# Kernel optimization log

Hardware: AMD Instinct MI355X
Metric: run time of the kernel (lower is better)

## Reference

```python
import jax, jax.numpy as jnp
import numpy as np

D_MODEL = 768
N_HEADS = 12
HEAD_DIM = D_MODEL // N_HEADS


def setup_inputs() -> dict:
    key = jax.random.key(0)
    ks = jax.random.split(key, 9)
    B, S = 2, 2048
    x = jax.random.normal(ks[0], (B, S, D_MODEL), dtype=jnp.float32)
    s = 1.0 / np.sqrt(D_MODEL)
    Wq = jax.random.normal(ks[1], (D_MODEL, D_MODEL), dtype=jnp.float32) * s
    bq = jax.random.normal(ks[2], (D_MODEL,), dtype=jnp.float32) * 0.01
    Wk = jax.random.normal(ks[3], (D_MODEL, D_MODEL), dtype=jnp.float32) * s
    bk = jax.random.normal(ks[4], (D_MODEL,), dtype=jnp.float32) * 0.01
    Wv = jax.random.normal(ks[5], (D_MODEL, D_MODEL), dtype=jnp.float32) * s
    bv = jax.random.normal(ks[6], (D_MODEL,), dtype=jnp.float32) * 0.01
    Wo = jax.random.normal(ks[7], (D_MODEL, D_MODEL), dtype=jnp.float32) * s
    bo = jax.random.normal(ks[8], (D_MODEL,), dtype=jnp.float32) * 0.01
    return {"x": x, "Wq": Wq, "bq": bq, "Wk": Wk, "bk": bk,
            "Wv": Wv, "bv": bv, "Wo": Wo, "bo": bo}


def reference(x, Wq, bq, Wk, bk, Wv, bv, Wo, bo):
    B, S, _ = x.shape
    H, Dh = N_HEADS, HEAD_DIM
    # Projections (torch Linear: x @ W.T + b; here W stored as [in, out])
    q = (x @ Wq + bq).reshape(B, S, H, Dh)
    k = (x @ Wk + bk).reshape(B, S, H, Dh)
    v = (x @ Wv + bv).reshape(B, S, H, Dh)
    scale = 1.0 / jnp.sqrt(jnp.float32(Dh))
    # NOTE: source applies no causal mask despite the class name.
    scores = jnp.einsum('bqhd,bkhd->bhqk', q, k) * scale
    attn = jax.nn.softmax(scores, axis=-1)
    out = jnp.einsum('bhqk,bkhd->bqhd', attn, v).reshape(B, S, H * Dh)
    return out @ Wo + bo
```

## Files before the change

kernel.cpp:

```cpp
#include <hip/hip_runtime.h>

typedef unsigned short u16;
typedef __fp16 halfx2 __attribute__((ext_vector_type(2)));
typedef __fp16 halfx8 __attribute__((ext_vector_type(8)));
typedef float floatx4 __attribute__((ext_vector_type(4)));
typedef unsigned short u16x4 __attribute__((ext_vector_type(4)));
typedef unsigned short u16x8 __attribute__((ext_vector_type(8)));

#define D_MODEL 768
#define NH 12
#define DH 64
#define SEQ 2048
#define BATCH 2
#define MTOK 4096
#define DQKV 2304

__device__ __forceinline__ u16 f2h(float f) {
    __fp16 h = (__fp16)f;
    return __builtin_bit_cast(u16, h);
}

__device__ __forceinline__ void gload_lds16(const void* g, void* l) {
    __builtin_amdgcn_global_load_lds(
        (const __attribute__((address_space(1))) void*)g,
        (__attribute__((address_space(3))) void*)l, 16, 0, 0);
}


__global__ __launch_bounds__(256) void wprep_kernel(const float* __restrict__ Wq, const float* __restrict__ Wk,
                                                    const float* __restrict__ Wv, const float* __restrict__ Wo,
                                                    const float* __restrict__ x,
                                                    u16* __restrict__ WqkvT, u16* __restrict__ WoT,
                                                    u16* __restrict__ xh) {
    __shared__ u16 t[64][72];
    int bid = blockIdx.x;
    int tid = threadIdx.x;
    if (bid >= 576) {
        int idx = (bid - 576) * 2048 + tid * 8;
        float4 v0 = *(const float4*)(x + idx);
        float4 v1 = *(const float4*)(x + idx + 4);
        union { u16x8 u; halfx2 h[4]; } pk;
        pk.h[0] = __builtin_amdgcn_cvt_pkrtz(v0.x, v0.y);
        pk.h[1] = __builtin_amdgcn_cvt_pkrtz(v0.z, v0.w);
        pk.h[2] = __builtin_amdgcn_cvt_pkrtz(v1.x, v1.y);
        pk.h[3] = __builtin_amdgcn_cvt_pkrtz(v1.z, v1.w);
        *(u16x8*)(xh + idx) = pk.u;
        return;
    }
    int z = bid / 144;
    int t2 = bid % 144;
    int k0 = (t2 / 12) * 64, n0 = (t2 % 12) * 64;
    const float* W = (z == 0) ? Wq : (z == 1) ? Wk : (z == 2) ? Wv : Wo;
    u16* dst = (z < 3) ? (WqkvT + (size_t)z * 768 * 768) : WoT;
#pragma unroll
    for (int p = 0; p < 16; ++p) {
        int idx = p * 256 + tid;
        int kr = idx >> 6, nc = idx & 63;
        t[kr][nc] = f2h(W[(size_t)(k0 + kr) * 768 + n0 + nc]);
    }
    __syncthreads();
#pragma unroll
    for (int p = 0; p < 16; ++p) {
        int idx = p * 256 + tid;
        int nr = idx >> 6, kc = idx & 63;
        dst[(size_t)(n0 + nr) * 768 + k0 + kc] = t[kc][nr];
    }
}


__global__ __launch_bounds__(256) void gemm_qkv(const u16* __restrict__ xh, const u16* __restrict__ Bt,
                                                const float* __restrict__ bq, const float* __restrict__ bk,
                                                const float* __restrict__ bv,
                                                u16* __restrict__ qP, u16* __restrict__ kP,
                                                u16* __restrict__ vTout) {
    const int tid = threadIdx.x;
    const int wid = tid >> 6;
    const int lane = tid & 63;
    const int qd = lane >> 4;
    const int l15 = lane & 15;

    const int tn = blockIdx.x * 128;
    const int tm = blockIdx.y * 64;
    const int wm = (wid >> 1) * 32;
    const int wn = (wid & 1) * 64;

    __shared__ alignas(16) u16 As[64 * 64];
    __shared__ alignas(16) u16 Bs[128 * 64];

    floatx4 acc[2][4];
#pragma unroll
    for (int i = 0; i < 2; ++i)
#pragma unroll
        for (int j = 0; j < 4; ++j) acc[i][j] = (floatx4)(0.0f);

    const u16* Ag[2];
#pragma unroll
    for (int rd = 0; rd < 2; ++rd) {
        int s = rd * 256 + tid;
        int r = s >> 3, bl = (s & 7) ^ (r & 7);
        Ag[rd] = xh + (size_t)(tm + r) * 768 + bl * 8;
    }
    const u16* Bg[4];
#pragma unroll
    for (int rd = 0; rd < 4; ++rd) {
        int s = rd * 256 + tid;
        int r = s >> 3, bl = (s & 7) ^ (r & 7);
        Bg[rd] = Bt + (size_t)(tn + r) * 768 + bl * 8;
    }

    for (int kb = 0; kb < 768; kb += 64) {
        __syncthreads();
#pragma unroll
        for (int rd = 0; rd < 2; ++rd)
            gload_lds16(Ag[rd] + kb, As + (size_t)(rd * 256 + tid) * 8);
#pragma unroll
        for (int rd = 0; rd < 4; ++rd)
            gload_lds16(Bg[rd] + kb, Bs + (size_t)(rd * 256 + tid) * 8);
        __syncthreads();

#pragma unroll
        for (int ks = 0; ks < 2; ++ks) {
            halfx8 af[2], bf[4];
#pragma unroll
            for (int i = 0; i < 2; ++i) {
                int r = wm + i * 16 + l15;
                af[i] = *(const halfx8*)(As + r * 64 + (((ks * 4 + qd) ^ (r & 7)) * 8));
            }
#pragma unroll
            for (int j = 0; j < 4; ++j) {
                int r2 = wn + j * 16 + l15;
                bf[j] = *(const halfx8*)(Bs + r2 * 64 + (((ks * 4 + qd) ^ (r2 & 7)) * 8));
            }
#pragma unroll
            for (int i = 0; i < 2; ++i)
#pragma unroll
                for (int j = 0; j < 4; ++j)
                    acc[i][j] = __builtin_amdgcn_mfma_f32_16x16x32_f16(af[i], bf[j], acc[i][j], 0, 0, 0);
        }
    }

    const float cscale = 0.125f * 1.44269504088896340736f;
    const int rgn = (tn < 768) ? 0 : (tn < 1536) ? 1 : 2;
    const float* bsrc = (rgn == 0) ? bq : (rgn == 1) ? bk : bv;
#pragma unroll
    for (int j = 0; j < 4; ++j) {
        int col = tn + wn + j * 16 + l15;
        int cl = col - rgn * 768;
        float bvv = bsrc[cl];
        int h = cl >> 6, d = cl & 63;
#pragma unroll
        for (int i = 0; i < 2; ++i) {
            int row0 = tm + wm + i * 16 + qd * 4;
            int b = row0 >> 11, s0 = row0 & 2047;
            u16x4 pk;
#pragma unroll
            for (int r = 0; r < 4; ++r) {
                float v = acc[i][j][r] + bvv;
                if (rgn == 0) v *= cscale;
                pk[r] = f2h(v);
            }
            if (rgn == 2) {
                *(u16x4*)(vTout + ((size_t)(b * NH + h) * 64 + d) * SEQ + s0) = pk;
            } else {
                u16* dst = (rgn == 0) ? qP : kP;
#pragma unroll
                for (int r = 0; r < 4; ++r)
                    dst[((size_t)(b * NH + h) * SEQ + s0 + r) * DH + d] = pk[r];
            }
        }
    }
}


__global__ __launch_bounds__(256, 2) void attn_kernel(const u16* __restrict__ qP, const u16* __restrict__ kP,
                                                      const u16* __restrict__ vT, u16* __restrict__ attn) {
    const int tid = threadIdx.x;
    const int wid = tid >> 6;
    const int lane = tid & 63;
    const int qd = lane >> 4;
    const int l15 = lane & 15;

    const int bh = blockIdx.x;
    const int b = bh / NH, h = bh % NH;
    const int q0 = blockIdx.y * 64;

    __shared__ alignas(16) u16 smem[9216];
    u16* ps = smem + wid * 2304;

    halfx8 aq[4][2];
#pragma unroll
    for (int jn = 0; jn < 4; ++jn)
#pragma unroll
        for (int ks = 0; ks < 2; ++ks)
            aq[jn][ks] = *(const halfx8*)(qP + (size_t)(bh * SEQ + q0 + jn * 16 + l15) * DH + ks * 32 + qd * 8);

    halfx8 ones;
#pragma unroll
    for (int j = 0; j < 8; ++j) ones[j] = (__fp16)1.0f;

    floatx4 o[4][4];
#pragma unroll
    for (int ip = 0; ip < 4; ++ip)
#pragma unroll
        for (int jn = 0; jn < 4; ++jn) o[ip][jn] = (floatx4)(0.0f);
    floatx4 lsum[4];
#pragma unroll
    for (int jn = 0; jn < 4; ++jn) lsum[jn] = (floatx4)(0.0f);

    const u16* kbase = kP + (size_t)(bh * SEQ + wid * 32 + l15) * DH + qd * 8;
    const u16* vbase = vT + (size_t)(bh * 64 + l15) * SEQ + wid * 32 + qd * 8;

    halfx8 avA[4], avB[4];
    floatx4 scA[2][4], scB[2][4];
    {
        halfx8 akp[2][2];
#pragma unroll
        for (int mi = 0; mi < 2; ++mi)
#pragma unroll
            for (int ks = 0; ks < 2; ++ks)
                akp[mi][ks] = *(const halfx8*)(kbase + (size_t)(mi * 16) * DH + ks * 32);
#pragma unroll
        for (int ip = 0; ip < 4; ++ip)
            avA[ip] = *(const halfx8*)(vbase + (size_t)(ip * 16) * SEQ);

#pragma unroll
        for (int mi = 0; mi < 2; ++mi)
#pragma unroll
            for (int jn = 0; jn < 4; ++jn) scA[mi][jn] = (floatx4)(0.0f);
#pragma unroll
        for (int ks = 0; ks < 2; ++ks)
#pragma unroll
            for (int mi = 0; mi < 2; ++mi)
#pragma unroll
                for (int jn = 0; jn < 4; ++jn)
                    scA[mi][jn] = __builtin_amdgcn_mfma_f32_16x16x32_f16(akp[mi][ks], aq[jn][ks], scA[mi][jn], 0, 0, 0);
    }

    auto body = [&](int kt,
                    floatx4 (&scC)[2][4], floatx4 (&scN)[2][4],
                    halfx8 (&avU)[4], halfx8 (&avF)[4]) {
        const int kt1 = (kt + 1) & 15;

        halfx8 akn[2][2];
#pragma unroll
        for (int mi = 0; mi < 2; ++mi)
#pragma unroll
            for (int ks = 0; ks < 2; ++ks)
                akn[mi][ks] = *(const halfx8*)(kbase + (size_t)(kt1 * 128 + mi * 16) * DH + ks * 32);
#pragma unroll
        for (int ip = 0; ip < 4; ++ip)
            avF[ip] = *(const halfx8*)(vbase + (size_t)(ip * 16) * SEQ + kt1 * 128);

#pragma unroll
        for (int mi = 0; mi < 2; ++mi)
#pragma unroll
            for (int jn = 0; jn < 4; ++jn) {
                float p0 = __builtin_amdgcn_exp2f(scC[mi][jn][0]);
                float p1 = __builtin_amdgcn_exp2f(scC[mi][jn][1]);
                float p2 = __builtin_amdgcn_exp2f(scC[mi][jn][2]);
                float p3 = __builtin_amdgcn_exp2f(scC[mi][jn][3]);
                union { u16x4 u; halfx2 h[2]; } pk;
                pk.h[0] = __builtin_amdgcn_cvt_pkrtz(p0, p1);
                pk.h[1] = __builtin_amdgcn_cvt_pkrtz(p2, p3);
                *(u16x4*)(ps + (jn * 16 + l15) * 36 + mi * 16 + qd * 4) = pk.u;
            }

#pragma unroll
        for (int mi = 0; mi < 2; ++mi)
#pragma unroll
            for (int jn = 0; jn < 4; ++jn) scN[mi][jn] = (floatx4)(0.0f);
        __builtin_amdgcn_s_setprio(1);
#pragma unroll
        for (int ks = 0; ks < 2; ++ks)
#pragma unroll
            for (int mi = 0; mi < 2; ++mi)
#pragma unroll
                for (int jn = 0; jn < 4; ++jn)
                    scN[mi][jn] = __builtin_amdgcn_mfma_f32_16x16x32_f16(akn[mi][ks], aq[jn][ks], scN[mi][jn], 0, 0, 0);
        __builtin_amdgcn_s_setprio(0);

        halfx8 bp[4];
#pragma unroll
        for (int jn = 0; jn < 4; ++jn) {
            union { halfx8 h8; u16x4 u4[2]; } bpu;
            bpu.u4[0] = *(const u16x4*)(ps + (jn * 16 + l15) * 36 + qd * 8);
            bpu.u4[1] = *(const u16x4*)(ps + (jn * 16 + l15) * 36 + qd * 8 + 4);
            bp[jn] = bpu.h8;
        }

        __builtin_amdgcn_s_setprio(1);
#pragma unroll
        for (int jn = 0; jn < 4; ++jn)
            lsum[jn] = __builtin_amdgcn_mfma_f32_16x16x32_f16(ones, bp[jn], lsum[jn], 0, 0, 0);
#pragma unroll
        for (int ip = 0; ip < 4; ++ip)
#pragma unroll
            for (int jn = 0; jn < 4; ++jn)
                o[ip][jn] = __builtin_amdgcn_mfma_f32_16x16x32_f16(avU[ip], bp[jn], o[ip][jn], 0, 0, 0);
        __builtin_amdgcn_s_setprio(0);
    };

    for (int kt = 0; kt < 16; kt += 2) {
        body(kt,     scA, scB, avA, avB);
        body(kt + 1, scB, scA, avB, avA);
    }

    float* Oacc = (float*)smem;
    float* la = (float*)smem + 4352;

    __syncthreads();
    if (wid == 0) {
#pragma unroll
        for (int jn = 0; jn < 4; ++jn) {
            int q = jn * 16 + l15;
#pragma unroll
            for (int ip = 0; ip < 4; ++ip)
                *(floatx4*)(Oacc + q * 68 + ip * 16 + qd * 4) = o[ip][jn];
            if (qd == 0) la[q] = lsum[jn][0];
        }
    }
    for (int w = 1; w < 4; ++w) {
        __syncthreads();
        if (wid == w) {
#pragma unroll
            for (int jn = 0; jn < 4; ++jn) {
                int q = jn * 16 + l15;
#pragma unroll
                for (int ip = 0; ip < 4; ++ip) {
                    float* p = Oacc + q * 68 + ip * 16 + qd * 4;
                    *(floatx4*)p = *(floatx4*)p + o[ip][jn];
                }
                if (qd == 0) la[q] += lsum[jn][0];
            }
        }
    }
    __syncthreads();

    {
        int q = tid >> 2, d0 = (tid & 3) * 16;
        float inv = __builtin_amdgcn_rcpf(la[q]);
        const float* op = Oacc + q * 68 + d0;
        u16x8 pk0, pk1;
#pragma unroll
        for (int r = 0; r < 8; ++r) pk0[r] = f2h(op[r] * inv);
#pragma unroll
        for (int r = 0; r < 8; ++r) pk1[r] = f2h(op[8 + r] * inv);
        u16* dst = attn + (size_t)(b * SEQ + q0 + q) * D_MODEL + h * DH + d0;
        *(u16x8*)dst = pk0;
        *(u16x8*)(dst + 8) = pk1;
    }
}


__global__ __launch_bounds__(256) void gemm_out(const u16* __restrict__ A, const u16* __restrict__ Bt,
                                                const float* __restrict__ bias, float* __restrict__ Cout) {
    const int tid = threadIdx.x;
    const int wid = tid >> 6;
    const int lane = tid & 63;
    const int qd = lane >> 4;
    const int l15 = lane & 15;

    const int tn = blockIdx.x * 64;
    const int tm = blockIdx.y * 64;
    const int wm = (wid >> 1) * 32;
    const int wn = (wid & 1) * 32;

    __shared__ alignas(16) u16 As[64 * 64];
    __shared__ alignas(16) u16 Bs[64 * 64];

    floatx4 acc[2][2];
#pragma unroll
    for (int i = 0; i < 2; ++i)
#pragma unroll
        for (int j = 0; j < 2; ++j) acc[i][j] = (floatx4)(0.0f);

    const u16* Ag[2];
    const u16* Bg[2];
#pragma unroll
    for (int rd = 0; rd < 2; ++rd) {
        int s = rd * 256 + tid;
        int r = s >> 3, bl = (s & 7) ^ (r & 7);
        Ag[rd] = A + (size_t)(tm + r) * 768 + bl * 8;
        Bg[rd] = Bt + (size_t)(tn + r) * 768 + bl * 8;
    }

    for (int kb = 0; kb < 768; kb += 64) {
        __syncthreads();
#pragma unroll
        for (int rd = 0; rd < 2; ++rd) {
            gload_lds16(Ag[rd] + kb, As + (size_t)(rd * 256 + tid) * 8);
            gload_lds16(Bg[rd] + kb, Bs + (size_t)(rd * 256 + tid) * 8);
        }
        __syncthreads();

#pragma unroll
        for (int ks = 0; ks < 2; ++ks) {
            halfx8 af[2], bf[2];
#pragma unroll
            for (int i = 0; i < 2; ++i) {
                int r = wm + i * 16 + l15;
                af[i] = *(const halfx8*)(As + r * 64 + (((ks * 4 + qd) ^ (r & 7)) * 8));
                int r2 = wn + i * 16 + l15;
                bf[i] = *(const halfx8*)(Bs + r2 * 64 + (((ks * 4 + qd) ^ (r2 & 7)) * 8));
            }
#pragma unroll
            for (int i = 0; i < 2; ++i)
#pragma unroll
                for (int j = 0; j < 2; ++j)
                    acc[i][j] = __builtin_amdgcn_mfma_f32_16x16x32_f16(af[i], bf[j], acc[i][j], 0, 0, 0);
        }
    }

#pragma unroll
    for (int j = 0; j < 2; ++j) {
        int col = tn + wn + j * 16 + l15;
        float bv = bias[col];
#pragma unroll
        for (int i = 0; i < 2; ++i) {
            int row0 = tm + wm + i * 16 + qd * 4;
#pragma unroll
            for (int r = 0; r < 4; ++r)
                Cout[(size_t)(row0 + r) * 768 + col] = acc[i][j][r] + bv;
        }
    }
}


extern "C" void kernel_launch(void* const* d_in, const int* in_sizes, int n_in,
                              void* d_out, int out_size, void* d_ws, size_t ws_size,
                              hipStream_t stream) {
    const float* x  = (const float*)d_in[0];
    const float* Wq = (const float*)d_in[1];
    const float* bq = (const float*)d_in[2];
    const float* Wk = (const float*)d_in[3];
    const float* bk = (const float*)d_in[4];
    const float* Wv = (const float*)d_in[5];
    const float* bv = (const float*)d_in[6];
    const float* Wo = (const float*)d_in[7];
    const float* bo = (const float*)d_in[8];

    char* ws = (char*)d_ws;
    size_t off = 0;
    auto take = [&](size_t bytes) -> char* {
        char* p = ws + off;
        off += (bytes + 255) & ~(size_t)255;
        return p;
    };
    u16* WqkvT = (u16*)take((size_t)DQKV * D_MODEL * 2);
    u16* WoT   = (u16*)take((size_t)D_MODEL * D_MODEL * 2);
    u16* qP    = (u16*)take((size_t)MTOK * D_MODEL * 2);
    u16* kP    = (u16*)take((size_t)MTOK * D_MODEL * 2);
    u16* vTb   = (u16*)take((size_t)BATCH * NH * DH * SEQ * 2);
    u16* attn  = (u16*)take((size_t)MTOK * D_MODEL * 2);
    u16* xh = attn;

    wprep_kernel<<<576 + (MTOK * D_MODEL / 2048), 256, 0, stream>>>(Wq, Wk, Wv, Wo, x, WqkvT, WoT, xh);
    gemm_qkv<<<dim3(DQKV / 128, MTOK / 64), 256, 0, stream>>>(xh, WqkvT, bq, bk, bv, qP, kP, vTb);
    attn_kernel<<<dim3(BATCH * NH, SEQ / 64), 256, 0, stream>>>(qP, kP, vTb, attn);
    gemm_out<<<dim3(D_MODEL / 64, MTOK / 64), 256, 0, stream>>>(attn, WoT, bo, (float*)d_out);
}
```

Baseline: 173.8 us.

## Cut attention register pressure to fit three blocks per CU

Raises the attention kernel's launch bounds from two to three blocks per CU. To free registers, the Q fragments move from registers into LDS and are reloaded for each MFMA. The double-buffered score and V registers are dropped, so V is now loaded in the same iteration it is used. The row sum is also accumulated in fp32 on the VALU with a cross-lane shuffle, replacing the extra MFMA against a ones vector. The risk is that V load latency and extra LDS reads are now exposed, and must be hidden by the higher occupancy.

```diff
diff --git a/kernel.cpp b/kernel.cpp
--- a/kernel.cpp
+++ b/kernel.cpp
@@ -172,7 +172,7 @@
 }
 
 
-__global__ __launch_bounds__(256, 2) void attn_kernel(const u16* __restrict__ qP, const u16* __restrict__ kP,
+__global__ __launch_bounds__(256, 3) void attn_kernel(const u16* __restrict__ qP, const u16* __restrict__ kP,
                                                       const u16* __restrict__ vT, u16* __restrict__ attn) {
     const int tid = threadIdx.x;
     const int wid = tid >> 6;
@@ -184,61 +184,52 @@
     const int b = bh / NH, h = bh % NH;
     const int q0 = blockIdx.y * 64;
 
-    __shared__ alignas(16) u16 smem[9216];
-    u16* ps = smem + wid * 2304;
-
-    halfx8 aq[4][2];
-#pragma unroll
-    for (int jn = 0; jn < 4; ++jn)
-#pragma unroll
-        for (int ks = 0; ks < 2; ++ks)
-            aq[jn][ks] = *(const halfx8*)(qP + (size_t)(bh * SEQ + q0 + jn * 16 + l15) * DH + ks * 32 + qd * 8);
-
-    halfx8 ones;
-#pragma unroll
-    for (int j = 0; j < 8; ++j) ones[j] = (__fp16)1.0f;
+    __shared__ alignas(16) u16 smem[13312];
+    u16* qlds = smem;
+    u16* ps = smem + 4096 + wid * 2304;
+
+#pragma unroll
+    for (int ks = 0; ks < 2; ++ks) {
+        halfx8 qv = *(const halfx8*)(qP + (size_t)(bh * SEQ + q0 + wid * 16 + l15) * DH + ks * 32 + qd * 8);
+        *(halfx8*)(qlds + (size_t)((ks * 4 + wid) * 64 + lane) * 8) = qv;
+    }
+    __syncthreads();
+
+    auto AQ = [&](int jn, int ks) -> halfx8 {
+        return *(const halfx8*)(qlds + (size_t)((ks * 4 + jn) * 64 + lane) * 8);
+    };
 
     floatx4 o[4][4];
 #pragma unroll
     for (int ip = 0; ip < 4; ++ip)
 #pragma unroll
         for (int jn = 0; jn < 4; ++jn) o[ip][jn] = (floatx4)(0.0f);
-    floatx4 lsum[4];
-#pragma unroll
-    for (int jn = 0; jn < 4; ++jn) lsum[jn] = (floatx4)(0.0f);
+    float lsum[4] = {0.0f, 0.0f, 0.0f, 0.0f};
 
     const u16* kbase = kP + (size_t)(bh * SEQ + wid * 32 + l15) * DH + qd * 8;
     const u16* vbase = vT + (size_t)(bh * 64 + l15) * SEQ + wid * 32 + qd * 8;
 
-    halfx8 avA[4], avB[4];
-    floatx4 scA[2][4], scB[2][4];
+    floatx4 sc[2][4];
     {
-        halfx8 akp[2][2];
+        halfx8 ak0[2][2];
 #pragma unroll
         for (int mi = 0; mi < 2; ++mi)
 #pragma unroll
             for (int ks = 0; ks < 2; ++ks)
-                akp[mi][ks] = *(const halfx8*)(kbase + (size_t)(mi * 16) * DH + ks * 32);
-#pragma unroll
-        for (int ip = 0; ip < 4; ++ip)
-            avA[ip] = *(const halfx8*)(vbase + (size_t)(ip * 16) * SEQ);
-
-#pragma unroll
-        for (int mi = 0; mi < 2; ++mi)
-#pragma unroll
-            for (int jn = 0; jn < 4; ++jn) scA[mi][jn] = (floatx4)(0.0f);
-#pragma unroll
-        for (int ks = 0; ks < 2; ++ks)
-#pragma unroll
-            for (int mi = 0; mi < 2; ++mi)
-#pragma unroll
-                for (int jn = 0; jn < 4; ++jn)
-                    scA[mi][jn] = __builtin_amdgcn_mfma_f32_16x16x32_f16(akp[mi][ks], aq[jn][ks], scA[mi][jn], 0, 0, 0);
-    }
-
-    auto body = [&](int kt,
-                    floatx4 (&scC)[2][4], floatx4 (&scN)[2][4],
-                    halfx8 (&avU)[4], halfx8 (&avF)[4]) {
+                ak0[mi][ks] = *(const halfx8*)(kbase + (size_t)(mi * 16) * DH + ks * 32);
+#pragma unroll
+        for (int jn = 0; jn < 4; ++jn) {
+            halfx8 a0 = AQ(jn, 0), a1 = AQ(jn, 1);
+#pragma unroll
+            for (int mi = 0; mi < 2; ++mi) {
+                floatx4 z = (floatx4)(0.0f);
+                z = __builtin_amdgcn_mfma_f32_16x16x32_f16(ak0[mi][0], a0, z, 0, 0, 0);
+                sc[mi][jn] = __builtin_amdgcn_mfma_f32_16x16x32_f16(ak0[mi][1], a1, z, 0, 0, 0);
+            }
+        }
+    }
+
+    for (int kt = 0; kt < 16; ++kt) {
         const int kt1 = (kt + 1) & 15;
 
         halfx8 akn[2][2];
@@ -247,62 +238,58 @@
 #pragma unroll
             for (int ks = 0; ks < 2; ++ks)
                 akn[mi][ks] = *(const halfx8*)(kbase + (size_t)(kt1 * 128 + mi * 16) * DH + ks * 32);
+        halfx8 avc[4];
 #pragma unroll
         for (int ip = 0; ip < 4; ++ip)
-            avF[ip] = *(const halfx8*)(vbase + (size_t)(ip * 16) * SEQ + kt1 * 128);
+            avc[ip] = *(const halfx8*)(vbase + (size_t)(ip * 16) * SEQ + kt * 128);
 
 #pragma unroll
         for (int mi = 0; mi < 2; ++mi)
 #pragma unroll
             for (int jn = 0; jn < 4; ++jn) {
-                float p0 = __builtin_amdgcn_exp2f(scC[mi][jn][0]);
-                float p1 = __builtin_amdgcn_exp2f(scC[mi][jn][1]);
-                float p2 = __builtin_amdgcn_exp2f(scC[mi][jn][2]);
-                float p3 = __builtin_amdgcn_exp2f(scC[mi][jn][3]);
+                float p0 = __builtin_amdgcn_exp2f(sc[mi][jn][0]);
+                float p1 = __builtin_amdgcn_exp2f(sc[mi][jn][1]);
+                float p2 = __builtin_amdgcn_exp2f(sc[mi][jn][2]);
+                float p3 = __builtin_amdgcn_exp2f(sc[mi][jn][3]);
+                lsum[jn] += (p0 + p1) + (p2 + p3);
                 union { u16x4 u; halfx2 h[2]; } pk;
                 pk.h[0] = __builtin_amdgcn_cvt_pkrtz(p0, p1);
                 pk.h[1] = __builtin_amdgcn_cvt_pkrtz(p2, p3);
                 *(u16x4*)(ps + (jn * 16 + l15) * 36 + mi * 16 + qd * 4) = pk.u;
             }
 
-#pragma unroll
-        for (int mi = 0; mi < 2; ++mi)
-#pragma unroll
-            for (int jn = 0; jn < 4; ++jn) scN[mi][jn] = (floatx4)(0.0f);
         __builtin_amdgcn_s_setprio(1);
 #pragma unroll
-        for (int ks = 0; ks < 2; ++ks)
-#pragma unroll
-            for (int mi = 0; mi < 2; ++mi)
-#pragma unroll
-                for (int jn = 0; jn < 4; ++jn)
-                    scN[mi][jn] = __builtin_amdgcn_mfma_f32_16x16x32_f16(akn[mi][ks], aq[jn][ks], scN[mi][jn], 0, 0, 0);
+        for (int jn = 0; jn < 4; ++jn) {
+            halfx8 a0 = AQ(jn, 0), a1 = AQ(jn, 1);
+#pragma unroll
+            for (int mi = 0; mi < 2; ++mi) {
+                floatx4 z = (floatx4)(0.0f);
+                z = __builtin_amdgcn_mfma_f32_16x16x32_f16(akn[mi][0], a0, z, 0, 0, 0);
+                sc[mi][jn] = __builtin_amdgcn_mfma_f32_16x16x32_f16(akn[mi][1], a1, z, 0, 0, 0);
+            }
+        }
         __builtin_amdgcn_s_setprio(0);
 
-        halfx8 bp[4];
 #pragma unroll
         for (int jn = 0; jn < 4; ++jn) {
             union { halfx8 h8; u16x4 u4[2]; } bpu;
             bpu.u4[0] = *(const u16x4*)(ps + (jn * 16 + l15) * 36 + qd * 8);
             bpu.u4[1] = *(const u16x4*)(ps + (jn * 16 + l15) * 36 + qd * 8 + 4);
-            bp[jn] = bpu.h8;
-        }
-
-        __builtin_amdgcn_s_setprio(1);
-#pragma unroll
-        for (int jn = 0; jn < 4; ++jn)
-            lsum[jn] = __builtin_amdgcn_mfma_f32_16x16x32_f16(ones, bp[jn], lsum[jn], 0, 0, 0);
-#pragma unroll
-        for (int ip = 0; ip < 4; ++ip)
-#pragma unroll
-            for (int jn = 0; jn < 4; ++jn)
-                o[ip][jn] = __builtin_amdgcn_mfma_f32_16x16x32_f16(avU[ip], bp[jn], o[ip][jn], 0, 0, 0);
-        __builtin_amdgcn_s_setprio(0);
-    };
-
-    for (int kt = 0; kt < 16; kt += 2) {
-        body(kt,     scA, scB, avA, avB);
-        body(kt + 1, scB, scA, avB, avA);
+            __builtin_amdgcn_s_setprio(1);
+#pragma unroll
+            for (int ip = 0; ip < 4; ++ip)
+                o[ip][jn] = __builtin_amdgcn_mfma_f32_16x16x32_f16(avc[ip], bpu.h8, o[ip][jn], 0, 0, 0);
+            __builtin_amdgcn_s_setprio(0);
+        }
+    }
+
+#pragma unroll
+    for (int jn = 0; jn < 4; ++jn) {
+        float v = lsum[jn];
+        v += __shfl_xor(v, 16, 64);
+        v += __shfl_xor(v, 32, 64);
+        lsum[jn] = v;
     }
 
     float* Oacc = (float*)smem;
@@ -316,7 +303,7 @@
 #pragma unroll
             for (int ip = 0; ip < 4; ++ip)
                 *(floatx4*)(Oacc + q * 68 + ip * 16 + qd * 4) = o[ip][jn];
-            if (qd == 0) la[q] = lsum[jn][0];
+            if (qd == 0) la[q] = lsum[jn];
         }
     }
     for (int w = 1; w < 4; ++w) {
@@ -330,7 +317,7 @@
                     float* p = Oacc + q * 68 + ip * 16 + qd * 4;
                     *(floatx4*)p = *(floatx4*)p + o[ip][jn];
                 }
-                if (qd == 0) la[q] += lsum[jn][0];
+                if (qd == 0) la[q] += lsum[jn];
             }
         }
     }
```

Result: slower. 197.5 us (+13.6%).
